# Performance work log

Hardware: AMD Instinct MI355X
Metric: run time of the kernel (lower is better)

## Reference

```python
import jax, jax.numpy as jnp
import numpy as np

EPS = 1e-12  # torch F.normalize eps

def setup_inputs() -> dict:
    key = jax.random.key(0)
    k1, k2, k3 = jax.random.split(key, 3)
    b, c, h, w = 4, 192, 128, 128
    x = jax.random.normal(k1, (b, c, h, w), dtype=jnp.float32)
    # torch Linear weight transposed: x @ W_qkv, columns ordered [q | k | v]
    W_qkv = jax.random.normal(k2, (c, 3 * c), dtype=jnp.float32) * (1.0 / np.sqrt(c))
    W_lin = jax.random.normal(k3, (c, c), dtype=jnp.float32) * (1.0 / np.sqrt(c))
    sigma = jnp.ones((1, 1), dtype=jnp.float32)
    return {"x": x, "W_qkv": W_qkv, "W_lin": W_lin, "sigma": sigma}

def _l2norm_tokens(t):
    # normalize along token axis (dim=1 of [b, hw, c]), torch-style eps clamp
    n = jnp.sqrt(jnp.sum(t * t, axis=1, keepdims=True))
    return t / jnp.maximum(n, EPS)

def reference(x, W_qkv, W_lin, sigma):
    b, c, h, w = x.shape
    xt = jnp.transpose(x.reshape(b, c, h * w), (0, 2, 1))  # [b, hw, c]
    qkv = xt @ W_qkv                                        # [b, hw, 3c]
    q, k, v = jnp.split(qkv, 3, axis=-1)
    q = _l2norm_tokens(q)
    k = _l2norm_tokens(k)
    attn = jnp.einsum('bnc,bnd->bcd', k, q) * sigma[0, 0]   # [b, c, c]
    attn = jax.nn.softmax(attn, axis=-1)
    out = jnp.einsum('bnc,bcd->bnd', v, attn) @ W_lin       # [b, hw, c]
    return jnp.transpose(out, (0, 2, 1)).reshape(b, c, h, w)
```

## Files before the change

kernel.cpp:

```cpp
#include <hip/hip_runtime.h>

#define CCH 192
#define HWN 16384
#define NB  4
#define SPLIT 16

typedef __attribute__((ext_vector_type(8))) short bf16x8;
typedef __attribute__((ext_vector_type(4))) float f32x4;


__device__ __forceinline__ ushort f2bf(float f) {
  union { float f; unsigned u; } v; v.f = f;
  return (ushort)((v.u + 0x7fffu + ((v.u >> 16) & 1u)) >> 16);
}

__device__ __forceinline__ float wsum(float v) {
#pragma unroll
  for (int off = 32; off > 0; off >>= 1) v += __shfl_xor(v, off, 64);
  return v;
}
__device__ __forceinline__ float wmax(float v) {
#pragma unroll
  for (int off = 32; off > 0; off >>= 1) v = fmaxf(v, __shfl_xor(v, off, 64));
  return v;
}

__global__ __launch_bounds__(256) void k0_wconv(const float* __restrict__ Wqkv, ushort* __restrict__ Wb) {
  int j0 = blockIdx.x * 64, c0 = blockIdx.y * 64;
  __shared__ float L[64][65];
  int t = threadIdx.x;
#pragma unroll
  for (int p = 0; p < 4; ++p) {
    int idx = t + 256 * p;
    int row = idx >> 4, col = (idx & 15) << 2;
    float4 v = *reinterpret_cast<const float4*>(&Wqkv[(size_t)(c0 + row) * 576 + j0 + col]);
    L[row][col] = v.x; L[row][col + 1] = v.y; L[row][col + 2] = v.z; L[row][col + 3] = v.w;
  }
  __syncthreads();
#pragma unroll
  for (int p = 0; p < 4; ++p) {
    int idx = t + 256 * p;
    int jrow = idx >> 4, c4 = (idx & 15) << 2;
    ushort4 o;
    o.x = f2bf(L[c4 + 0][jrow]);
    o.y = f2bf(L[c4 + 1][jrow]);
    o.z = f2bf(L[c4 + 2][jrow]);
    o.w = f2bf(L[c4 + 3][jrow]);
    *reinterpret_cast<ushort4*>(&Wb[(size_t)(j0 + jrow) * CCH + c0 + c4]) = o;
  }
}

__global__ __launch_bounds__(256, 4) void k12_qkv(
    const float* __restrict__ x, const ushort* __restrict__ Wb,
    ushort* __restrict__ Tqk2, ushort* __restrict__ Vt2, float* __restrict__ norm2p)
{
  int z = blockIdx.z;
  const float* xb = x + (size_t)z * CCH * HWN;
  ushort* Tb2 = Tqk2 + (size_t)z * 384 * HWN;
  ushort* Vb2 = Vt2 + (size_t)z * HWN * CCH;
  float* npb = norm2p + (size_t)z * 256 * 384;
  int jt = blockIdx.x;
  int nt = blockIdx.y;
  int n0 = nt * 64;
  __shared__ __align__(16) ushort SM[13056];
  ushort* FR = SM;
  int t = threadIdx.x, l = t & 63, w = t >> 6;
  int lg = l >> 4, lr = l & 15;

  {
    int nl = l;
    const float* xrow = xb + n0 + nl;
    int frbase = (nl >> 4) * 3072 + (nl & 15) * 8;
#pragma unroll
    for (int tile = 0; tile < 6; ++tile) {
      int chunk = tile * 4 + w;
      int c0 = chunk * 8;
      float v[8];
#pragma unroll
      for (int j = 0; j < 8; ++j)
        v[j] = xrow[(size_t)(c0 + j) * HWN];
      unsigned q0 = (unsigned)f2bf(v[0]) | ((unsigned)f2bf(v[1]) << 16);
      unsigned q1 = (unsigned)f2bf(v[2]) | ((unsigned)f2bf(v[3]) << 16);
      unsigned q2 = (unsigned)f2bf(v[4]) | ((unsigned)f2bf(v[5]) << 16);
      unsigned q3 = (unsigned)f2bf(v[6]) | ((unsigned)f2bf(v[7]) << 16);
      *reinterpret_cast<int4*>(&FR[frbase + chunk * 128]) = make_int4(q0, q1, q2, q3);
    }
  }
  __syncthreads();

  f32x4 acc[4][3] = {};
#pragma unroll
  for (int k = 0; k < 6; ++k) {
    bf16x8 a[4], b[3];
#pragma unroll
    for (int m = 0; m < 4; ++m)
      a[m] = *reinterpret_cast<const bf16x8*>(&FR[m * 3072 + (4 * k + lg) * 128 + lr * 8]);
#pragma unroll
    for (int f = 0; f < 3; ++f)
      b[f] = *reinterpret_cast<const bf16x8*>(
          &Wb[(size_t)(jt * 192 + w * 48 + 16 * f + lr) * CCH + 32 * k + 8 * lg]);
#pragma unroll
    for (int m = 0; m < 4; ++m)
#pragma unroll
      for (int f = 0; f < 3; ++f)
        acc[m][f] = __builtin_amdgcn_mfma_f32_16x16x32_bf16(a[m], b[f], acc[m][f], 0, 0, 0);
  }
  __syncthreads();

  if (jt == 2) {
    ushort* Ep = SM;
#pragma unroll
    for (int m = 0; m < 4; ++m)
#pragma unroll
      for (int f = 0; f < 3; ++f) {
        int cl = w * 48 + 16 * f + lr;
        int nb = 16 * m + 4 * lg;
#pragma unroll
        for (int r = 0; r < 4; ++r)
          Ep[(nb + r) * 200 + cl] = f2bf(acc[m][f][r]);
      }
    __syncthreads();
    int nblk = n0 >> 4;
#pragma unroll
    for (int p = 0; p < 6; ++p) {
      int ii = t + 256 * p;
      int nq = ii & 15, n16 = ii / 384, cg = (ii - n16 * 384) >> 4;
      int4 v = *reinterpret_cast<const int4*>(&Ep[(n16 * 16 + nq) * 200 + cg * 8]);
      size_t off = (size_t)(nblk + n16) * (16 * CCH) + cg * 128 + nq * 8;
      *reinterpret_cast<int4*>(&Vb2[off]) = v;
    }
  } else {
#pragma unroll
    for (int f = 0; f < 3; ++f) {
      float sq = 0.f;
#pragma unroll
      for (int m = 0; m < 4; ++m)
#pragma unroll
        for (int r = 0; r < 4; ++r) sq += acc[m][f][r] * acc[m][f][r];
      sq += __shfl_xor(sq, 16, 64);
      sq += __shfl_xor(sq, 32, 64);
      if (lg == 0) {
        int j = jt * 192 + w * 48 + 16 * f + lr;
        npb[(size_t)nt * 384 + j] = sq;
      }
    }
    ushort* Ep = SM;
#pragma unroll
    for (int m = 0; m < 4; ++m)
#pragma unroll
      for (int f = 0; f < 3; ++f) {
        int jl = w * 48 + 16 * f + lr;
        int nb = 16 * m + 4 * lg;
        unsigned p0 = (unsigned)f2bf(acc[m][f][0]) | ((unsigned)f2bf(acc[m][f][1]) << 16);
        unsigned p1 = (unsigned)f2bf(acc[m][f][2]) | ((unsigned)f2bf(acc[m][f][3]) << 16);
        *reinterpret_cast<unsigned*>(&Ep[jl * 68 + nb]) = p0;
        *reinterpret_cast<unsigned*>(&Ep[jl * 68 + nb + 2]) = p1;
      }
    __syncthreads();
#pragma unroll
    for (int p = 0; p < 6; ++p) {
      int ii = t + 256 * p;
      int jq = ii & 15, nc = (ii >> 4) & 7, jb16 = ii >> 7;
      int4 v = *reinterpret_cast<const int4*>(&Ep[(jb16 * 16 + jq) * 68 + nc * 8]);
      size_t off = (size_t)(jt * 12 + jb16) * (16 * HWN) + ((size_t)(n0 >> 3) + nc) * 128 + jq * 8;
      *reinterpret_cast<int4*>(&Tb2[off]) = v;
    }
  }
}

__global__ __launch_bounds__(256) void k3_invn(const float* __restrict__ norm2p, float* __restrict__ invn) {
  int z = blockIdx.y, j = blockIdx.x;
  const float* npb = norm2p + (size_t)z * 256 * 384;
  int t = threadIdx.x;
  float s = npb[(size_t)t * 384 + j];
  s = wsum(s);
  __shared__ float red[4];
  if ((t & 63) == 0) red[t >> 6] = s;
  __syncthreads();
  if (t == 0) {
    float tot = red[0] + red[1] + red[2] + red[3];
    invn[(size_t)z * 384 + j] = 1.f / fmaxf(sqrtf(tot), 1e-12f);
  }
}

__global__ __launch_bounds__(256) void k4_gram(const ushort* __restrict__ Tqk2, float* __restrict__ Gpart) {
  int z = blockIdx.z;
  const ushort* Tb2 = Tqk2 + (size_t)z * 384 * HWN;
  float* Gb = Gpart + (size_t)z * SPLIT * CCH * CCH;
  int tile = blockIdx.x, chunk = blockIdx.y;
  int ct = tile / 3, dt = tile % 3;
  int t = threadIdx.x, l = t & 63, w = t >> 6;
  int wc = w >> 1, wd = w & 1, lg = l >> 4, lr = l & 15;
  f32x4 acc[2][2] = {};
  for (int s = 0; s < 16; ++s) {
    int nco = chunk * 128 + s * 8;
#pragma unroll
    for (int hh = 0; hh < 2; ++hh) {
      int ko = nco + 4 * hh + lg;
      bf16x8 a[2], bb[2];
#pragma unroll
      for (int m = 0; m < 2; ++m)
        a[m] = *reinterpret_cast<const bf16x8*>(
            &Tb2[(size_t)(12 + 4 * ct + 2 * wc + m) * (16 * HWN) + (size_t)ko * 128 + lr * 8]);
#pragma unroll
      for (int f = 0; f < 2; ++f)
        bb[f] = *reinterpret_cast<const bf16x8*>(
            &Tb2[(size_t)(4 * dt + 2 * wd + f) * (16 * HWN) + (size_t)ko * 128 + lr * 8]);
#pragma unroll
      for (int m = 0; m < 2; ++m)
#pragma unroll
        for (int f = 0; f < 2; ++f)
          acc[m][f] = __builtin_amdgcn_mfma_f32_16x16x32_bf16(a[m], bb[f], acc[m][f], 0, 0, 0);
    }
  }
#pragma unroll
  for (int m = 0; m < 2; ++m)
#pragma unroll
    for (int f = 0; f < 2; ++f)
#pragma unroll
      for (int r = 0; r < 4; ++r)
        Gb[(size_t)(chunk * CCH + ct * 64 + 32 * wc + 16 * m + 4 * lg + r) * CCH +
           dt * 64 + 32 * wd + 16 * f + lr] = acc[m][f][r];
}

__global__ __launch_bounds__(64) void k5_softmax(
    const float* __restrict__ Gpart, const float* __restrict__ invn,
    const float* __restrict__ sigma, float* __restrict__ S)
{
  int c = blockIdx.x, z = blockIdx.y;
  const float* Gb = Gpart + (size_t)z * SPLIT * CCH * CCH;
  const float* inb = invn + (size_t)z * 384;
  float sig = sigma[0];
  float ink = inb[192 + c];
  float lv[3];
#pragma unroll
  for (int r = 0; r < 3; ++r) {
    int d = threadIdx.x + 64 * r;
    float s = 0.f;
    for (int ch = 0; ch < SPLIT; ++ch)
      s += Gb[(size_t)(ch * CCH + c) * CCH + d];
    lv[r] = s * ink * inb[d] * sig;
  }
  float m = fmaxf(lv[0], fmaxf(lv[1], lv[2]));
  m = wmax(m);
  float e[3], tot = 0.f;
#pragma unroll
  for (int r = 0; r < 3; ++r) { e[r] = __expf(lv[r] - m); tot += e[r]; }
  tot = wsum(tot);
  float inv = 1.f / tot;
  float* Sb = S + (size_t)z * CCH * CCH;
#pragma unroll
  for (int r = 0; r < 3; ++r) Sb[(size_t)c * CCH + threadIdx.x + 64 * r] = e[r] * inv;
}

__global__ __launch_bounds__(192) void k6_mlin(
    const float* __restrict__ S, const float* __restrict__ Wlin, ushort* __restrict__ Mt)
{
  int z = blockIdx.y, c = blockIdx.x, e = threadIdx.x;
  const float* Sb = S + (size_t)z * CCH * CCH;
  float s = 0.f;
  for (int d = 0; d < CCH; ++d) s += Sb[(size_t)c * CCH + d] * Wlin[(size_t)d * CCH + e];
  Mt[(size_t)z * CCH * CCH + (size_t)e * CCH + c] = f2bf(s);
}

__global__ __launch_bounds__(256, 2) void k7_out(
    const ushort* __restrict__ Mt, const ushort* __restrict__ Vt2, float* __restrict__ out)
{
  int z = blockIdx.z;
  const ushort* Mb = Mt + (size_t)z * CCH * CCH;
  const ushort* Vb2 = Vt2 + (size_t)z * HWN * CCH;
  float* ob = out + (size_t)z * CCH * HWN;
  int nt = blockIdx.x, et = blockIdx.y;
  int e0 = et * 64, n0 = nt * 128;
  int t = threadIdx.x, l = t & 63, w = t >> 6;
  int wn = w >> 1, we = w & 1, lg = l >> 4, lr = l & 15;
  int nblk = n0 >> 4;
  bf16x8 mfrag[2][3][2];
#pragma unroll
  for (int h = 0; h < 2; ++h)
#pragma unroll
    for (int k3 = 0; k3 < 3; ++k3)
#pragma unroll
      for (int mg = 0; mg < 2; ++mg)
        mfrag[h][k3][mg] = *reinterpret_cast<const bf16x8*>(
            &Mb[(size_t)(e0 + 32 * we + 16 * mg + lr) * CCH + 96 * h + 32 * k3 + 8 * lg]);
  f32x4 acc[4][2] = {};
#pragma unroll
  for (int h = 0; h < 2; ++h)
#pragma unroll
    for (int k3 = 0; k3 < 3; ++k3) {
      bf16x8 an[4];
#pragma unroll
      for (int ng = 0; ng < 4; ++ng)
        an[ng] = *reinterpret_cast<const bf16x8*>(
            &Vb2[(size_t)(nblk + 4 * wn + ng) * (16 * CCH) + (12 * h + 4 * k3 + lg) * 128 + lr * 8]);
#pragma unroll
      for (int ng = 0; ng < 4; ++ng)
#pragma unroll
        for (int mg = 0; mg < 2; ++mg)
          acc[ng][mg] = __builtin_amdgcn_mfma_f32_16x16x32_bf16(an[ng], mfrag[h][k3][mg], acc[ng][mg], 0, 0, 0);
    }
#pragma unroll
  for (int ng = 0; ng < 4; ++ng)
#pragma unroll
    for (int mg = 0; mg < 2; ++mg)
      *reinterpret_cast<f32x4*>(
          &ob[(size_t)(e0 + 32 * we + 16 * mg + lr) * HWN + n0 + 64 * wn + 16 * ng + 4 * lg]) = acc[ng][mg];
}

extern "C" void kernel_launch(void* const* d_in, const int* in_sizes, int n_in,
                              void* d_out, int out_size, void* d_ws, size_t ws_size,
                              hipStream_t stream) {
  const float* x     = (const float*)d_in[0];
  const float* Wqkv  = (const float*)d_in[1];
  const float* Wlin  = (const float*)d_in[2];
  const float* sigma = (const float*)d_in[3];
  float* out = (float*)d_out;

  const size_t wbElems = (size_t)576 * CCH;
  const size_t perB =
      (size_t)384 * HWN * 2 +
      (size_t)HWN * CCH * 2 +
      (size_t)256 * 384 * 4 +
      (size_t)384 * 4 +
      (size_t)SPLIT * CCH * CCH * 4 +
      (size_t)CCH * CCH * 4 +
      (size_t)CCH * CCH * 2;
  int per = (ws_size >= wbElems * 2 + (size_t)NB * perB) ? NB : 1;

  ushort* Wb = (ushort*)d_ws;
  k0_wconv<<<dim3(9, 3), 256, 0, stream>>>(Wqkv, Wb);

  for (int b0 = 0; b0 < NB; b0 += per) {
    char* base = (char*)d_ws + wbElems * 2;
    ushort* Tqk2 = (ushort*)base;
    ushort* Vt2  = Tqk2 + (size_t)per * 384 * HWN;
    float* norm2p = (float*)(Vt2 + (size_t)per * HWN * CCH);
    float* invn  = norm2p + (size_t)per * 256 * 384;
    float* Gpart = invn + (size_t)per * 384;
    float* S     = Gpart + (size_t)per * SPLIT * CCH * CCH;
    ushort* Mt   = (ushort*)(S + (size_t)per * CCH * CCH);
    const float* xb = x + (size_t)b0 * CCH * HWN;
    float* ob = out + (size_t)b0 * CCH * HWN;

    k12_qkv   <<<dim3(3, 256, per), 256, 0, stream>>>(xb, Wb, Tqk2, Vt2, norm2p);
    k3_invn   <<<dim3(384, per), 256, 0, stream>>>(norm2p, invn);
    k4_gram   <<<dim3(9, SPLIT, per), 256, 0, stream>>>(Tqk2, Gpart);
    k5_softmax<<<dim3(192, per), 64, 0, stream>>>(Gpart, invn, sigma, S);
    k6_mlin   <<<dim3(192, per), 192, 0, stream>>>(S, Wlin, Mt);
    k7_out    <<<dim3(128, 3, per), 256, 0, stream>>>(Mt, Vt2, ob);
  }
}
```

Baseline: 119.8 us.

## Fold output-column tiles into QKV and output kernels to reuse loaded inputs

The QKV projection kernel now loops over all three column tiles (q, k, v) inside one block, so each 64-token slice of x is read from global memory, converted to bf16 and held in registers once rather than three times. The output kernel likewise loops over all three 64-wide output-channel tiles per block, reusing each V fragment load for three tiles. This removes redundant global reads and bf16 conversions but cuts grid size threefold, raises register pressure (a[6][4] fragments, acc[3][4][2]) and lowers the occupancy hint for k12 from 4 to 2. It may reduce parallelism and latency hiding on a many-CU device.

```diff
diff --git a/kernel.cpp b/kernel.cpp
--- a/kernel.cpp
+++ b/kernel.cpp
@@ -50,17 +50,16 @@
   }
 }
 
-__global__ __launch_bounds__(256, 4) void k12_qkv(
+__global__ __launch_bounds__(256, 2) void k12_qkv(
     const float* __restrict__ x, const ushort* __restrict__ Wb,
     ushort* __restrict__ Tqk2, ushort* __restrict__ Vt2, float* __restrict__ norm2p)
 {
-  int z = blockIdx.z;
+  int z = blockIdx.y;
   const float* xb = x + (size_t)z * CCH * HWN;
   ushort* Tb2 = Tqk2 + (size_t)z * 384 * HWN;
   ushort* Vb2 = Vt2 + (size_t)z * HWN * CCH;
   float* npb = norm2p + (size_t)z * 256 * 384;
-  int jt = blockIdx.x;
-  int nt = blockIdx.y;
+  int nt = blockIdx.x;
   int n0 = nt * 64;
   __shared__ __align__(16) ushort SM[13056];
   ushort* FR = SM;
@@ -88,83 +87,91 @@
   }
   __syncthreads();
 
-  f32x4 acc[4][3] = {};
-#pragma unroll
-  for (int k = 0; k < 6; ++k) {
-    bf16x8 a[4], b[3];
+  bf16x8 a[6][4];
+#pragma unroll
+  for (int k = 0; k < 6; ++k)
 #pragma unroll
     for (int m = 0; m < 4; ++m)
-      a[m] = *reinterpret_cast<const bf16x8*>(&FR[m * 3072 + (4 * k + lg) * 128 + lr * 8]);
-#pragma unroll
-    for (int f = 0; f < 3; ++f)
-      b[f] = *reinterpret_cast<const bf16x8*>(
-          &Wb[(size_t)(jt * 192 + w * 48 + 16 * f + lr) * CCH + 32 * k + 8 * lg]);
-#pragma unroll
-    for (int m = 0; m < 4; ++m)
+      a[k][m] = *reinterpret_cast<const bf16x8*>(&FR[m * 3072 + (4 * k + lg) * 128 + lr * 8]);
+  __syncthreads();
+
+#pragma unroll
+  for (int jt = 0; jt < 3; ++jt) {
+    f32x4 acc[4][3] = {};
+#pragma unroll
+    for (int k = 0; k < 6; ++k) {
+      bf16x8 b[3];
 #pragma unroll
       for (int f = 0; f < 3; ++f)
-        acc[m][f] = __builtin_amdgcn_mfma_f32_16x16x32_bf16(a[m], b[f], acc[m][f], 0, 0, 0);
-  }
-  __syncthreads();
-
-  if (jt == 2) {
-    ushort* Ep = SM;
-#pragma unroll
-    for (int m = 0; m < 4; ++m)
+        b[f] = *reinterpret_cast<const bf16x8*>(
+            &Wb[(size_t)(jt * 192 + w * 48 + 16 * f + lr) * CCH + 32 * k + 8 * lg]);
+#pragma unroll
+      for (int m = 0; m < 4; ++m)
+#pragma unroll
+        for (int f = 0; f < 3; ++f)
+          acc[m][f] = __builtin_amdgcn_mfma_f32_16x16x32_bf16(a[k][m], b[f], acc[m][f], 0, 0, 0);
+    }
+
+    if (jt == 2) {
+      ushort* Ep = SM;
+#pragma unroll
+      for (int m = 0; m < 4; ++m)
+#pragma unroll
+        for (int f = 0; f < 3; ++f) {
+          int cl = w * 48 + 16 * f + lr;
+          int nb = 16 * m + 4 * lg;
+#pragma unroll
+          for (int r = 0; r < 4; ++r)
+            Ep[(nb + r) * 200 + cl] = f2bf(acc[m][f][r]);
+        }
+      __syncthreads();
+      int nblk = n0 >> 4;
+#pragma unroll
+      for (int p = 0; p < 6; ++p) {
+        int ii = t + 256 * p;
+        int nq = ii & 15, n16 = ii / 384, cg = (ii - n16 * 384) >> 4;
+        int4 v = *reinterpret_cast<const int4*>(&Ep[(n16 * 16 + nq) * 200 + cg * 8]);
+        size_t off = (size_t)(nblk + n16) * (16 * CCH) + cg * 128 + nq * 8;
+        *reinterpret_cast<int4*>(&Vb2[off]) = v;
+      }
+    } else {
 #pragma unroll
       for (int f = 0; f < 3; ++f) {
-        int cl = w * 48 + 16 * f + lr;
-        int nb = 16 * m + 4 * lg;
-#pragma unroll
-        for (int r = 0; r < 4; ++r)
-          Ep[(nb + r) * 200 + cl] = f2bf(acc[m][f][r]);
+        float sq = 0.f;
+#pragma unroll
+        for (int m = 0; m < 4; ++m)
+#pragma unroll
+          for (int r = 0; r < 4; ++r) sq += acc[m][f][r] * acc[m][f][r];
+        sq += __shfl_xor(sq, 16, 64);
+        sq += __shfl_xor(sq, 32, 64);
+        if (lg == 0) {
+          int j = jt * 192 + w * 48 + 16 * f + lr;
+          npb[(size_t)nt * 384 + j] = sq;
+        }
       }
+      ushort* Ep = SM;
+#pragma unroll
+      for (int m = 0; m < 4; ++m)
+#pragma unroll
+        for (int f = 0; f < 3; ++f) {
+          int jl = w * 48 + 16 * f + lr;
+          int nb = 16 * m + 4 * lg;
+          unsigned p0 = (unsigned)f2bf(acc[m][f][0]) | ((unsigned)f2bf(acc[m][f][1]) << 16);
+          unsigned p1 = (unsigned)f2bf(acc[m][f][2]) | ((unsigned)f2bf(acc[m][f][3]) << 16);
+          *reinterpret_cast<unsigned*>(&Ep[jl * 68 + nb]) = p0;
+          *reinterpret_cast<unsigned*>(&Ep[jl * 68 + nb + 2]) = p1;
+        }
+      __syncthreads();
+#pragma unroll
+      for (int p = 0; p < 6; ++p) {
+        int ii = t + 256 * p;
+        int jq = ii & 15, nc = (ii >> 4) & 7, jb16 = ii >> 7;
+        int4 v = *reinterpret_cast<const int4*>(&Ep[(jb16 * 16 + jq) * 68 + nc * 8]);
+        size_t off = (size_t)(jt * 12 + jb16) * (16 * HWN) + ((size_t)(n0 >> 3) + nc) * 128 + jq * 8;
+        *reinterpret_cast<int4*>(&Tb2[off]) = v;
+      }
+    }
     __syncthreads();
-    int nblk = n0 >> 4;
-#pragma unroll
-    for (int p = 0; p < 6; ++p) {
-      int ii = t + 256 * p;
-      int nq = ii & 15, n16 = ii / 384, cg = (ii - n16 * 384) >> 4;
-      int4 v = *reinterpret_cast<const int4*>(&Ep[(n16 * 16 + nq) * 200 + cg * 8]);
-      size_t off = (size_t)(nblk + n16) * (16 * CCH) + cg * 128 + nq * 8;
-      *reinterpret_cast<int4*>(&Vb2[off]) = v;
-    }
-  } else {
-#pragma unroll
-    for (int f = 0; f < 3; ++f) {
-      float sq = 0.f;
-#pragma unroll
-      for (int m = 0; m < 4; ++m)
-#pragma unroll
-        for (int r = 0; r < 4; ++r) sq += acc[m][f][r] * acc[m][f][r];
-      sq += __shfl_xor(sq, 16, 64);
-      sq += __shfl_xor(sq, 32, 64);
-      if (lg == 0) {
-        int j = jt * 192 + w * 48 + 16 * f + lr;
-        npb[(size_t)nt * 384 + j] = sq;
-      }
-    }
-    ushort* Ep = SM;
-#pragma unroll
-    for (int m = 0; m < 4; ++m)
-#pragma unroll
-      for (int f = 0; f < 3; ++f) {
-        int jl = w * 48 + 16 * f + lr;
-        int nb = 16 * m + 4 * lg;
-        unsigned p0 = (unsigned)f2bf(acc[m][f][0]) | ((unsigned)f2bf(acc[m][f][1]) << 16);
-        unsigned p1 = (unsigned)f2bf(acc[m][f][2]) | ((unsigned)f2bf(acc[m][f][3]) << 16);
-        *reinterpret_cast<unsigned*>(&Ep[jl * 68 + nb]) = p0;
-        *reinterpret_cast<unsigned*>(&Ep[jl * 68 + nb + 2]) = p1;
-      }
-    __syncthreads();
-#pragma unroll
-    for (int p = 0; p < 6; ++p) {
-      int ii = t + 256 * p;
-      int jq = ii & 15, nc = (ii >> 4) & 7, jb16 = ii >> 7;
-      int4 v = *reinterpret_cast<const int4*>(&Ep[(jb16 * 16 + jq) * 68 + nc * 8]);
-      size_t off = (size_t)(jt * 12 + jb16) * (16 * HWN) + ((size_t)(n0 >> 3) + nc) * 128 + jq * 8;
-      *reinterpret_cast<int4*>(&Tb2[off]) = v;
-    }
   }
 }
 
@@ -266,25 +273,16 @@
 __global__ __launch_bounds__(256, 2) void k7_out(
     const ushort* __restrict__ Mt, const ushort* __restrict__ Vt2, float* __restrict__ out)
 {
-  int z = blockIdx.z;
+  int z = blockIdx.y;
   const ushort* Mb = Mt + (size_t)z * CCH * CCH;
   const ushort* Vb2 = Vt2 + (size_t)z * HWN * CCH;
   float* ob = out + (size_t)z * CCH * HWN;
-  int nt = blockIdx.x, et = blockIdx.y;
-  int e0 = et * 64, n0 = nt * 128;
+  int nt = blockIdx.x;
+  int n0 = nt * 128;
   int t = threadIdx.x, l = t & 63, w = t >> 6;
   int wn = w >> 1, we = w & 1, lg = l >> 4, lr = l & 15;
   int nblk = n0 >> 4;
-  bf16x8 mfrag[2][3][2];
-#pragma unroll
-  for (int h = 0; h < 2; ++h)
-#pragma unroll
-    for (int k3 = 0; k3 < 3; ++k3)
-#pragma unroll
-      for (int mg = 0; mg < 2; ++mg)
-        mfrag[h][k3][mg] = *reinterpret_cast<const bf16x8*>(
-            &Mb[(size_t)(e0 + 32 * we + 16 * mg + lr) * CCH + 96 * h + 32 * k3 + 8 * lg]);
-  f32x4 acc[4][2] = {};
+  f32x4 acc[3][4][2] = {};
 #pragma unroll
   for (int h = 0; h < 2; ++h)
 #pragma unroll
@@ -295,17 +293,27 @@
         an[ng] = *reinterpret_cast<const bf16x8*>(
             &Vb2[(size_t)(nblk + 4 * wn + ng) * (16 * CCH) + (12 * h + 4 * k3 + lg) * 128 + lr * 8]);
 #pragma unroll
-      for (int ng = 0; ng < 4; ++ng)
+      for (int et = 0; et < 3; ++et) {
+        bf16x8 mf[2];
 #pragma unroll
         for (int mg = 0; mg < 2; ++mg)
-          acc[ng][mg] = __builtin_amdgcn_mfma_f32_16x16x32_bf16(an[ng], mfrag[h][k3][mg], acc[ng][mg], 0, 0, 0);
-    }
-#pragma unroll
-  for (int ng = 0; ng < 4; ++ng)
-#pragma unroll
-    for (int mg = 0; mg < 2; ++mg)
-      *reinterpret_cast<f32x4*>(
-          &ob[(size_t)(e0 + 32 * we + 16 * mg + lr) * HWN + n0 + 64 * wn + 16 * ng + 4 * lg]) = acc[ng][mg];
+          mf[mg] = *reinterpret_cast<const bf16x8*>(
+              &Mb[(size_t)(et * 64 + 32 * we + 16 * mg + lr) * CCH + 96 * h + 32 * k3 + 8 * lg]);
+#pragma unroll
+        for (int ng = 0; ng < 4; ++ng)
+#pragma unroll
+          for (int mg = 0; mg < 2; ++mg)
+            acc[et][ng][mg] = __builtin_amdgcn_mfma_f32_16x16x32_bf16(an[ng], mf[mg], acc[et][ng][mg], 0, 0, 0);
+      }
+    }
+#pragma unroll
+  for (int et = 0; et < 3; ++et)
+#pragma unroll
+    for (int ng = 0; ng < 4; ++ng)
+#pragma unroll
+      for (int mg = 0; mg < 2; ++mg)
+        *reinterpret_cast<f32x4*>(
+            &ob[(size_t)(et * 64 + 32 * we + 16 * mg + lr) * HWN + n0 + 64 * wn + 16 * ng + 4 * lg]) = acc[et][ng][mg];
 }
 
 extern "C" void kernel_launch(void* const* d_in, const int* in_sizes, int n_in,
@@ -343,11 +351,11 @@
     const float* xb = x + (size_t)b0 * CCH * HWN;
     float* ob = out + (size_t)b0 * CCH * HWN;
 
-    k12_qkv   <<<dim3(3, 256, per), 256, 0, stream>>>(xb, Wb, Tqk2, Vt2, norm2p);
+    k12_qkv   <<<dim3(256, per), 256, 0, stream>>>(xb, Wb, Tqk2, Vt2, norm2p);
     k3_invn   <<<dim3(384, per), 256, 0, stream>>>(norm2p, invn);
     k4_gram   <<<dim3(9, SPLIT, per), 256, 0, stream>>>(Tqk2, Gpart);
     k5_softmax<<<dim3(192, per), 64, 0, stream>>>(Gpart, invn, sigma, S);
     k6_mlin   <<<dim3(192, per), 192, 0, stream>>>(S, Wlin, Mt);
-    k7_out    <<<dim3(128, 3, per), 256, 0, stream>>>(Mt, Vt2, ob);
-  }
-}
+    k7_out    <<<dim3(128, per), 256, 0, stream>>>(Mt, Vt2, ob);
+  }
+}
```

Result: faster. 116.3 us (-3.0%).
